# Performance work log

Hardware: AMD Instinct MI355X
Metric: run time of the kernel (lower is better)

## Reference

```python
import jax, jax.numpy as jnp
import numpy as np
from jax import lax

B, C, OUT, K, H, W = 8, 64, 32, 3, 64, 64


def _conv2d(x, w, b, stride=1, pad=0, groups=1):
    o = lax.conv_general_dilated(x, w, (stride, stride), [(pad, pad), (pad, pad)],
                                 dimension_numbers=('NCHW', 'OIHW', 'NCHW'),
                                 feature_group_count=groups)
    return o + b[None, :, None, None]


def _bn(x, g, b, m, v, eps=1e-5):
    # eval-mode BatchNorm2d with running stats
    s = g / jnp.sqrt(v + eps)
    return x * s[None, :, None, None] + (b - m * s)[None, :, None, None]


def _eca(x, w):
    # global avg pool -> 1D conv over channel axis -> sigmoid gate [b,c,1,1]
    y = x.mean((-2, -1))[:, None, :]  # [b,1,c]
    y = lax.conv_general_dilated(y, w, (1,), [(1, 1)],
                                 dimension_numbers=('NCW', 'OIW', 'NCW'))
    return jax.nn.sigmoid(y[:, 0, :])[:, :, None, None]


def _avgpool3(x):
    # AvgPool2d(k=3, stride=1, pad=1), count_include_pad=True (torch default)
    s = lax.reduce_window(x, 0.0, lax.add, (1, 1, 3, 3), (1, 1, 1, 1),
                          [(0, 0), (0, 0), (1, 1), (1, 1)])
    return s / 9.0


def _forward(x, sc_w, sc_b, ac_w, ac_b, oc_w, oc_b, oc_bn_g, oc_bn_b, oc_bn_m, oc_bn_v,
             ex_w, ey_w, ez_w, ff_w, ff_b, g1_w, g1_b, g2_w, g2_b,
             fu_w, fu_b, fu_bn_g, fu_bn_b, fu_bn_m, fu_bn_v):
    b, c, h, w = x.shape
    k = K
    # --- ReceptiveFieldAttentionConv ---
    frf = jax.nn.silu(_conv2d(x, sc_w, sc_b, pad=k // 2, groups=c))
    frf = frf.reshape(b, c, k * k, h, w)
    arf = _conv2d(_avgpool3(x), ac_w, ac_b, groups=c).reshape(b, c, k * k, h, w)
    arf = jax.nn.softmax(arf, axis=2)  # softmax over k*k RF positions
    wt = (frf * arf).reshape(b, c, k, k, h, w)
    wt = wt.transpose(0, 1, 4, 2, 5, 3).reshape(b, c, h * k, w * k)  # pixel-shuffle-like
    x_rfa = jax.nn.silu(_bn(_conv2d(wt, oc_w, oc_b, stride=k, groups=4),
                            oc_bn_g, oc_bn_b, oc_bn_m, oc_bn_v))
    # --- FrequencyGroupedChannelAttention ---
    energy = jnp.abs(jnp.fft.fft2(x)).mean((-2, -1))  # [b,c]
    ranks = jnp.argsort(jnp.argsort(-energy, axis=1), axis=1)
    mask = (ranks < c // 2).astype(x.dtype)[:, :, None, None]  # top-half-energy channels
    a_x = _eca(x, ex_w)
    a_y = _eca(x * mask, ey_w)
    a_z = _eca(x * (1.0 - mask), ez_w)
    a_f = _conv2d(jnp.concatenate([a_y, a_z], 1), ff_w, ff_b, groups=4)
    g_in = jnp.concatenate([a_f, a_x], 1)
    g = jax.nn.sigmoid(_conv2d(jax.nn.silu(_conv2d(g_in, g1_w, g1_b)), g2_w, g2_b))
    x_fgca = x * (g * a_f + (1.0 - g) * a_x)
    # --- fuse ---
    fused = jnp.concatenate([x_rfa, x_fgca], 1)
    return jax.nn.silu(_bn(_conv2d(fused, fu_w, fu_b),
                           fu_bn_g, fu_bn_b, fu_bn_m, fu_bn_v))


def setup_inputs() -> dict:
    key = jax.random.key(0)
    ks = jax.random.split(key, 32)
    rn = lambda k, shp, s=0.1: jax.random.normal(k, shp, jnp.float32) * s
    gh = max(8, C // 4)  # gate hidden = 16
    return {
        'x': jax.random.normal(ks[0], (B, C, H, W), jnp.float32),
        'sc_w': rn(ks[1], (C * K * K, 1, K, K)), 'sc_b': rn(ks[2], (C * K * K,)),
        'ac_w': rn(ks[3], (C * K * K, 1, 1, 1)), 'ac_b': rn(ks[4], (C * K * K,)),
        'oc_w': rn(ks[5], (C, C // 4, K, K)), 'oc_b': rn(ks[6], (C,)),
        'oc_bn_g': 1.0 + rn(ks[7], (C,)), 'oc_bn_b': rn(ks[8], (C,)),
        'oc_bn_m': rn(ks[9], (C,)), 'oc_bn_v': 0.9 + 0.2 * jax.random.uniform(ks[10], (C,), jnp.float32),
        'ex_w': rn(ks[11], (1, 1, 3), 0.3), 'ey_w': rn(ks[12], (1, 1, 3), 0.3),
        'ez_w': rn(ks[13], (1, 1, 3), 0.3),
        'ff_w': rn(ks[14], (C, 2 * C // 4, 1, 1)), 'ff_b': rn(ks[15], (C,)),
        'g1_w': rn(ks[16], (gh, 2 * C, 1, 1)), 'g1_b': rn(ks[17], (gh,)),
        'g2_w': rn(ks[18], (C, gh, 1, 1)), 'g2_b': rn(ks[19], (C,)),
        'fu_w': rn(ks[20], (OUT, 2 * C, 1, 1)), 'fu_b': rn(ks[21], (OUT,)),
        'fu_bn_g': 1.0 + rn(ks[22], (OUT,)), 'fu_bn_b': rn(ks[23], (OUT,)),
        'fu_bn_m': rn(ks[24], (OUT,)), 'fu_bn_v': 0.9 + 0.2 * jax.random.uniform(ks[25], (OUT,), jnp.float32),
    }


def reference(x, sc_w, sc_b, ac_w, ac_b, oc_w, oc_b, oc_bn_g, oc_bn_b, oc_bn_m, oc_bn_v,
              ex_w, ey_w, ez_w, ff_w, ff_b, g1_w, g1_b, g2_w, g2_b,
              fu_w, fu_b, fu_bn_g, fu_bn_b, fu_bn_m, fu_bn_v):
    return _forward(x, sc_w, sc_b, ac_w, ac_b, oc_w, oc_b, oc_bn_g, oc_bn_b, oc_bn_m, oc_bn_v,
                    ex_w, ey_w, ez_w, ff_w, ff_b, g1_w, g1_b, g2_w, g2_b,
                    fu_w, fu_b, fu_bn_g, fu_bn_b, fu_bn_m, fu_bn_v)
```

## Files before the change

kernel.cpp:

```cpp
#include <hip/hip_runtime.h>
#include <math.h>

#define EPS 1e-5f

__device__ __forceinline__ float wave_sum(float v) {
  v += __shfl_down(v, 32);
  v += __shfl_down(v, 16);
  v += __shfl_down(v, 8);
  v += __shfl_down(v, 4);
  v += __shfl_down(v, 2);
  v += __shfl_down(v, 1);
  return v;
}

__device__ __forceinline__ float silu_f(float v) { return v / (1.f + __expf(-v)); }
__device__ __forceinline__ float sigm_f(float v) { return 1.f / (1.f + __expf(-v)); }

__device__ __forceinline__ int bitrev6(int v) {
  return ((v & 1) << 5) | ((v & 2) << 3) | ((v & 4) << 1) |
         ((v & 8) >> 1) | ((v & 16) >> 3) | ((v & 32) >> 5);
}

#define FFT6(zr, zi)                                           \
  do {                                                         \
    _Pragma("unroll") for (int s = 0; s < 6; ++s) {            \
      const int half = 32 >> s;                                \
      const bool up = (lane & half) != 0;                      \
      float pr = __shfl_xor(zr, half);                         \
      float pi = __shfl_xor(zi, half);                         \
      float tr = up ? pr - zr : zr + pr;                       \
      float ti = up ? pi - zi : zi + pi;                       \
      const float c = twc[s], sn = tws[s];                     \
      zr = tr * c - ti * sn;                                   \
      zi = tr * sn + ti * c;                                   \
    }                                                          \
  } while (0)

__global__ __launch_bounds__(256) void k_dft(const float* __restrict__ x,
                                             float* __restrict__ energy,
                                             float* __restrict__ meanx) {
  __shared__ float re1[33 * 65];
  __shared__ float im1[33 * 65];
  __shared__ float redA[4], redB[4];
  const int bc = blockIdx.x;
  const int tid = threadIdx.x;
  const int lane = tid & 63;
  const int wv = tid >> 6;
  const float* xp = x + (size_t)bc * 4096;

  float twc[6], tws[6];
#pragma unroll
  for (int s = 0; s < 6; ++s) {
    int half = 32 >> s;
    if (lane & half) {
      float ang = -6.283185307179586f * (float)((lane & (half - 1)) << s) / 64.f;
      float sv, cv;
      __sincosf(ang, &sv, &cv);
      twc[s] = cv;
      tws[s] = sv;
    } else {
      twc[s] = 1.f;
      tws[s] = 0.f;
    }
  }

  const int f = bitrev6(lane);
  const int fm = (64 - f) & 63;
  const int plane = bitrev6(fm);

  float lsum = 0.f;
#pragma unroll 1
  for (int rp = 0; rp < 4; ++rp) {
    const int h0 = wv * 16 + rp * 4;
    float x0 = xp[h0 * 64 + lane];
    float x1 = xp[(h0 + 1) * 64 + lane];
    float x2 = xp[(h0 + 2) * 64 + lane];
    float x3 = xp[(h0 + 3) * 64 + lane];
    lsum += x0 + x1 + x2 + x3;
    float zr = x0, zi = x1, yr = x2, yi = x3;
#pragma unroll
    for (int s = 0; s < 6; ++s) {
      const int half = 32 >> s;
      const bool up = (lane & half) != 0;
      float pzr = __shfl_xor(zr, half);
      float pzi = __shfl_xor(zi, half);
      float pyr = __shfl_xor(yr, half);
      float pyi = __shfl_xor(yi, half);
      float tzr = up ? pzr - zr : zr + pzr;
      float tzi = up ? pzi - zi : zi + pzi;
      float tyr = up ? pyr - yr : yr + pyr;
      float tyi = up ? pyi - yi : yi + pyi;
      const float c = twc[s], sn = tws[s];
      zr = tzr * c - tzi * sn;
      zi = tzr * sn + tzi * c;
      yr = tyr * c - tyi * sn;
      yi = tyr * sn + tyi * c;
    }
    float mzr = __shfl(zr, plane), mzi = __shfl(zi, plane);
    float myr = __shfl(yr, plane), myi = __shfl(yi, plane);
    if (f <= 32) {
      float ar = 0.5f * (zr + mzr), ai = 0.5f * (zi - mzi);
      float br = 0.5f * (zi + mzi), bi = 0.5f * (mzr - zr);
      float cr = 0.5f * (yr + myr), ci = 0.5f * (yi - myi);
      float dr = 0.5f * (yi + myi), di = 0.5f * (myr - yr);
      re1[f * 65 + h0] = ar;     im1[f * 65 + h0] = ai;
      re1[f * 65 + h0 + 1] = br; im1[f * 65 + h0 + 1] = bi;
      re1[f * 65 + h0 + 2] = cr; im1[f * 65 + h0 + 2] = ci;
      re1[f * 65 + h0 + 3] = dr; im1[f * 65 + h0 + 3] = di;
    }
  }
  __syncthreads();

  float msum = 0.f;
#pragma unroll 1
  for (int i = 0; i < 4; ++i) {
    const int kv1 = wv + 8 * i;
    const int kv2 = kv1 + 4;
    const float w1 = (kv1 == 0) ? 1.f : 2.f;
    float ar = re1[kv1 * 65 + lane];
    float ai = im1[kv1 * 65 + lane];
    float br = re1[kv2 * 65 + lane];
    float bi = im1[kv2 * 65 + lane];
#pragma unroll
    for (int s = 0; s < 6; ++s) {
      const int half = 32 >> s;
      const bool up = (lane & half) != 0;
      float par = __shfl_xor(ar, half);
      float pai = __shfl_xor(ai, half);
      float pbr = __shfl_xor(br, half);
      float pbi = __shfl_xor(bi, half);
      float tar = up ? par - ar : ar + par;
      float tai = up ? pai - ai : ai + pai;
      float tbr = up ? pbr - br : br + pbr;
      float tbi = up ? pbi - bi : bi + pbi;
      const float c = twc[s], sn = tws[s];
      ar = tar * c - tai * sn;
      ai = tar * sn + tai * c;
      br = tbr * c - tbi * sn;
      bi = tbr * sn + tbi * c;
    }
    msum += w1 * sqrtf(ar * ar + ai * ai) + 2.f * sqrtf(br * br + bi * bi);
  }
  if (wv == 0) {
    float ar = re1[32 * 65 + lane];
    float ai = im1[32 * 65 + lane];
    FFT6(ar, ai);
    msum += sqrtf(ar * ar + ai * ai);
  }

  msum = wave_sum(msum);
  lsum = wave_sum(lsum);
  if (lane == 0) { redA[wv] = msum; redB[wv] = lsum; }
  __syncthreads();
  if (tid == 0) {
    float e = redA[0] + redA[1] + redA[2] + redA[3];
    float m = redB[0] + redB[1] + redB[2] + redB[3];
    energy[bc] = e * (1.f / 4096.f);
    meanx[bc] = m * (1.f / 4096.f);
  }
}

__global__ __launch_bounds__(64) void k_attn(
    const float* __restrict__ energy, const float* __restrict__ meanx,
    const float* __restrict__ ex_w, const float* __restrict__ ey_w,
    const float* __restrict__ ez_w, const float* __restrict__ ff_w,
    const float* __restrict__ ff_b, const float* __restrict__ g1_w,
    const float* __restrict__ g1_b, const float* __restrict__ g2_w,
    const float* __restrict__ g2_b, float* __restrict__ s2) {
  __shared__ float e[64], mx[64], my[64], mz[64];
  __shared__ float ax[64], ay[64], az[64], af[64], h1[16];
  const int b = blockIdx.x;
  const int c = threadIdx.x;
  e[c] = energy[b * 64 + c];
  mx[c] = meanx[b * 64 + c];
  __syncthreads();
  int rank = 0;
  float ec = e[c];
  for (int i = 0; i < 64; ++i) {
    float ei = e[i];
    rank += (ei > ec) || (ei == ec && i < c);
  }
  float mask = (rank < 32) ? 1.f : 0.f;
  my[c] = mx[c] * mask;
  mz[c] = mx[c] * (1.f - mask);
  __syncthreads();
  {
    float l, r, m;
    l = (c > 0) ? mx[c - 1] : 0.f; m = mx[c]; r = (c < 63) ? mx[c + 1] : 0.f;
    ax[c] = sigm_f(ex_w[0] * l + ex_w[1] * m + ex_w[2] * r);
    l = (c > 0) ? my[c - 1] : 0.f; m = my[c]; r = (c < 63) ? my[c + 1] : 0.f;
    ay[c] = sigm_f(ey_w[0] * l + ey_w[1] * m + ey_w[2] * r);
    l = (c > 0) ? mz[c - 1] : 0.f; m = mz[c]; r = (c < 63) ? mz[c + 1] : 0.f;
    az[c] = sigm_f(ez_w[0] * l + ez_w[1] * m + ez_w[2] * r);
  }
  __syncthreads();
  {
    int g = c >> 4;
    float acc = ff_b[c];
#pragma unroll
    for (int i = 0; i < 32; ++i) {
      int ch = g * 32 + i;
      float v = (ch < 64) ? ay[ch] : az[ch - 64];
      acc = fmaf(v, ff_w[c * 32 + i], acc);
    }
    af[c] = acc;
  }
  __syncthreads();
  if (c < 16) {
    float a = g1_b[c];
#pragma unroll
    for (int i = 0; i < 64; ++i) a = fmaf(af[i], g1_w[c * 128 + i], a);
#pragma unroll
    for (int i = 0; i < 64; ++i) a = fmaf(ax[i], g1_w[c * 128 + 64 + i], a);
    h1[c] = silu_f(a);
  }
  __syncthreads();
  float gv = g2_b[c];
#pragma unroll
  for (int o = 0; o < 16; ++o) gv = fmaf(h1[o], g2_w[c * 16 + o], gv);
  gv = sigm_f(gv);
  s2[b * 64 + c] = gv * af[c] + (1.f - gv) * ax[c];
}

__global__ __launch_bounds__(256) void k_rfa(
    const float* __restrict__ x,
    const float* __restrict__ sc_w, const float* __restrict__ sc_b,
    const float* __restrict__ ac_w, const float* __restrict__ ac_b,
    const float* __restrict__ oc_w, const float* __restrict__ oc_b,
    const float* __restrict__ bn_g, const float* __restrict__ bn_b,
    const float* __restrict__ bn_m, const float* __restrict__ bn_v,
    float* __restrict__ xrfa) {
  __shared__ __align__(16) float scwp[16 * 9 * 12];
  __shared__ __align__(16) float mp[16 * 24];
  __shared__ __align__(16) float ocwp[16 * 16 * 12];
  __shared__ float red[128 * 33];
  const int blk = blockIdx.x;
  const int band = blk & 15;
  const int g = (blk >> 4) & 3;
  const int b = blk >> 6;
  const int tid = threadIdx.x;
  const int lane = tid & 63;
  const int wv = tid >> 6;
  const int wp = wv & 1;
  const int half = wv >> 1;

  for (int i = tid; i < 1296; i += 256) {
    int icg = i / 81, rem = i - icg * 81;
    int j = rem / 9, t = rem - j * 9;
    scwp[icg * 108 + j * 12 + t] = sc_w[(g * 144 + icg * 9 + j) * 9 + t];
  }
  if (tid < 144) {
    int icg = tid / 9, j = tid - icg * 9;
    scwp[icg * 108 + j * 12 + 9] = sc_b[g * 144 + tid];
    mp[icg * 24 + j] = ac_w[g * 144 + tid];
    mp[icg * 24 + 12 + j] = ac_b[g * 144 + tid];
  }
  for (int i = tid; i < 2304; i += 256) {
    int oco = i / 144, rem = i - oco * 144;
    int icg = rem / 9, j = rem - icg * 9;
    ocwp[icg * 192 + oco * 12 + j] = oc_w[((g * 16 + oco) * 16 + icg) * 9 + j];
  }
  __syncthreads();

  const int r0 = band * 4 + wp * 2;
  const int w = lane;
  const bool vW = w > 0, vE = w < 63;
  float acc0[16], acc1[16];
#pragma unroll
  for (int i = 0; i < 16; ++i) { acc0[i] = 0.f; acc1[i] = 0.f; }

  const float* xg = x + ((size_t)(b * 64 + g * 16)) * 4096 + w;
  const int icg0 = half * 8;

#pragma unroll 1
  for (int ii = 0; ii < 8; ++ii) {
    const int icg = icg0 + ii;
    const float* xc = xg + icg * 4096;
    float n[12];
#pragma unroll
    for (int t = 0; t < 4; ++t) {
      int h = r0 - 1 + t;
      bool vh = (h >= 0) && (h < 64);
      const float* row = xc + h * 64;
      n[t * 3 + 0] = (vh && vW) ? row[-1] : 0.f;
      n[t * 3 + 1] = vh ? row[0] : 0.f;
      n[t * 3 + 2] = (vh && vE) ? row[1] : 0.f;
    }
    float rs0 = n[0] + n[1] + n[2];
    float rs1 = n[3] + n[4] + n[5];
    float rs2 = n[6] + n[7] + n[8];
    float rs3 = n[9] + n[10] + n[11];
    float ap0 = (rs0 + rs1 + rs2) * (1.f / 9.f);
    float ap1 = (rs1 + rs2 + rs3) * (1.f / 9.f);

    float aw[12], ab[12];
    *(float4*)&aw[0] = *(const float4*)&mp[icg * 24];
    *(float4*)&aw[4] = *(const float4*)&mp[icg * 24 + 4];
    *(float4*)&aw[8] = *(const float4*)&mp[icg * 24 + 8];
    *(float4*)&ab[0] = *(const float4*)&mp[icg * 24 + 12];
    *(float4*)&ab[4] = *(const float4*)&mp[icg * 24 + 16];
    *(float4*)&ab[8] = *(const float4*)&mp[icg * 24 + 20];

    float f0[9], f1[9], a0[9], a1[9];
    float amax0 = -1e30f, amax1 = -1e30f;
#pragma unroll
    for (int j = 0; j < 9; ++j) {
      float wt[12];
      *(float4*)&wt[0] = *(const float4*)&scwp[icg * 108 + j * 12];
      *(float4*)&wt[4] = *(const float4*)&scwp[icg * 108 + j * 12 + 4];
      *(float4*)&wt[8] = *(const float4*)&scwp[icg * 108 + j * 12 + 8];
      float p0 = wt[9], p1 = wt[9];
#pragma unroll
      for (int t = 0; t < 9; ++t) {
        p0 = fmaf(n[t], wt[t], p0);
        p1 = fmaf(n[t + 3], wt[t], p1);
      }
      f0[j] = silu_f(p0);
      f1[j] = silu_f(p1);
      float v0 = fmaf(ap0, aw[j], ab[j]);
      float v1 = fmaf(ap1, aw[j], ab[j]);
      a0[j] = v0; a1[j] = v1;
      amax0 = fmaxf(amax0, v0);
      amax1 = fmaxf(amax1, v1);
    }
    float es0 = 0.f, es1 = 0.f;
    float p0[9], p1[9];
#pragma unroll
    for (int j = 0; j < 9; ++j) {
      float e0 = __expf(a0[j] - amax0);
      float e1 = __expf(a1[j] - amax1);
      es0 += e0; es1 += e1;
      p0[j] = f0[j] * e0;
      p1[j] = f1[j] * e1;
    }
    float i0 = __fdividef(1.f, es0);
    float i1 = __fdividef(1.f, es1);
#pragma unroll
    for (int j = 0; j < 9; ++j) { p0[j] *= i0; p1[j] *= i1; }

#pragma unroll
    for (int oco = 0; oco < 16; ++oco) {
      float ov[12];
      *(float4*)&ov[0] = *(const float4*)&ocwp[icg * 192 + oco * 12];
      *(float4*)&ov[4] = *(const float4*)&ocwp[icg * 192 + oco * 12 + 4];
      *(float4*)&ov[8] = *(const float4*)&ocwp[icg * 192 + oco * 12 + 8];
      float s0 = 0.f, s1 = 0.f;
#pragma unroll
      for (int j = 0; j < 9; ++j) {
        s0 = fmaf(p0[j], ov[j], s0);
        s1 = fmaf(p1[j], ov[j], s1);
      }
      acc0[oco] += s0;
      acc1[oco] += s1;
    }
  }

  const int rid = wp * 64 + lane;
  if (half == 1) {
#pragma unroll
    for (int k = 0; k < 16; ++k) {
      red[rid * 33 + k] = acc0[k];
      red[rid * 33 + 16 + k] = acc1[k];
    }
  }
  __syncthreads();
  if (half == 0) {
#pragma unroll
    for (int k = 0; k < 16; ++k) {
      acc0[k] += red[rid * 33 + k];
      acc1[k] += red[rid * 33 + 16 + k];
    }
    float* op = xrfa + ((size_t)(b * 64 + g * 16)) * 4096 + r0 * 64 + w;
#pragma unroll
    for (int oco = 0; oco < 16; ++oco) {
      int oc = g * 16 + oco;
      float s = bn_g[oc] * rsqrtf(bn_v[oc] + EPS);
      float bb = bn_b[oc] - bn_m[oc] * s;
      float ob = oc_b[oc];
      float v0 = fmaf(acc0[oco] + ob, s, bb);
      float v1 = fmaf(acc1[oco] + ob, s, bb);
      op[oco * 4096] = silu_f(v0);
      op[oco * 4096 + 64] = silu_f(v1);
    }
  }
}

__global__ __launch_bounds__(256) void k_fuse(
    const float* __restrict__ x, const float* __restrict__ xrfa,
    const float* __restrict__ s2, const float* __restrict__ fu_w,
    const float* __restrict__ fu_b, const float* __restrict__ bn_g,
    const float* __restrict__ bn_b, const float* __restrict__ bn_m,
    const float* __restrict__ bn_v, float* __restrict__ out) {
  __shared__ __align__(16) float fw[4096];
  __shared__ float s2l[64];
  const int blk = blockIdx.x;
  const int tid = threadIdx.x;
  const int sloc = tid & 63;
  const int ocq = tid >> 6;
  const int b = blk >> 6;
  const int sp = (blk & 63) * 64 + sloc;

  for (int i = tid; i < 1024; i += 256)
    ((float4*)fw)[i] = ((const float4*)fu_w)[i];
  if (tid < 64) s2l[tid] = s2[b * 64 + tid];

  const float* xr = xrfa + (size_t)b * 64 * 4096 + sp;
  const float* xp = x + (size_t)b * 64 * 4096 + sp;
  float va[64], vb[64];
#pragma unroll
  for (int i = 0; i < 64; ++i) va[i] = xr[i * 4096];
#pragma unroll
  for (int i = 0; i < 64; ++i) vb[i] = xp[i * 4096];
  __syncthreads();
#pragma unroll
  for (int i = 0; i < 64; ++i) vb[i] *= s2l[i];

  float* op = out + (size_t)b * 32 * 4096 + sp;
#pragma unroll 1
  for (int o = 0; o < 8; ++o) {
    const int oc = ocq * 8 + o;
    const float* wr = &fw[oc * 128];
    float a = 0.f;
#pragma unroll
    for (int q = 0; q < 16; ++q) {
      float4 w4 = *(const float4*)&wr[q * 4];
      a = fmaf(va[q * 4 + 0], w4.x, a);
      a = fmaf(va[q * 4 + 1], w4.y, a);
      a = fmaf(va[q * 4 + 2], w4.z, a);
      a = fmaf(va[q * 4 + 3], w4.w, a);
    }
#pragma unroll
    for (int q = 0; q < 16; ++q) {
      float4 w4 = *(const float4*)&wr[64 + q * 4];
      a = fmaf(vb[q * 4 + 0], w4.x, a);
      a = fmaf(vb[q * 4 + 1], w4.y, a);
      a = fmaf(vb[q * 4 + 2], w4.z, a);
      a = fmaf(vb[q * 4 + 3], w4.w, a);
    }
    float s = bn_g[oc] * rsqrtf(bn_v[oc] + EPS);
    float v = a + fu_b[oc];
    v = fmaf(v, s, bn_b[oc] - bn_m[oc] * s);
    op[oc * 4096] = silu_f(v);
  }
}

extern "C" void kernel_launch(void* const* d_in, const int* in_sizes, int n_in,
                              void* d_out, int out_size, void* d_ws, size_t ws_size,
                              hipStream_t stream) {
  const float* x       = (const float*)d_in[0];
  const float* sc_w    = (const float*)d_in[1];
  const float* sc_b    = (const float*)d_in[2];
  const float* ac_w    = (const float*)d_in[3];
  const float* ac_b    = (const float*)d_in[4];
  const float* oc_w    = (const float*)d_in[5];
  const float* oc_b    = (const float*)d_in[6];
  const float* oc_bn_g = (const float*)d_in[7];
  const float* oc_bn_b = (const float*)d_in[8];
  const float* oc_bn_m = (const float*)d_in[9];
  const float* oc_bn_v = (const float*)d_in[10];
  const float* ex_w    = (const float*)d_in[11];
  const float* ey_w    = (const float*)d_in[12];
  const float* ez_w    = (const float*)d_in[13];
  const float* ff_w    = (const float*)d_in[14];
  const float* ff_b    = (const float*)d_in[15];
  const float* g1_w    = (const float*)d_in[16];
  const float* g1_b    = (const float*)d_in[17];
  const float* g2_w    = (const float*)d_in[18];
  const float* g2_b    = (const float*)d_in[19];
  const float* fu_w    = (const float*)d_in[20];
  const float* fu_b    = (const float*)d_in[21];
  const float* fu_bn_g = (const float*)d_in[22];
  const float* fu_bn_b = (const float*)d_in[23];
  const float* fu_bn_m = (const float*)d_in[24];
  const float* fu_bn_v = (const float*)d_in[25];

  float* ws     = (float*)d_ws;
  float* energy = ws;
  float* meanx  = ws + 512;
  float* s2     = ws + 1024;
  float* xrfa   = ws + 2048;

  k_dft<<<512, 256, 0, stream>>>(x, energy, meanx);
  k_attn<<<8, 64, 0, stream>>>(energy, meanx, ex_w, ey_w, ez_w,
                               ff_w, ff_b, g1_w, g1_b, g2_w, g2_b, s2);
  k_rfa<<<512, 256, 0, stream>>>(x, sc_w, sc_b, ac_w, ac_b, oc_w, oc_b,
                                 oc_bn_g, oc_bn_b, oc_bn_m, oc_bn_v, xrfa);
  k_fuse<<<512, 256, 0, stream>>>(x, xrfa, s2, fu_w, fu_b,
                                  fu_bn_g, fu_bn_b, fu_bn_m, fu_bn_v,
                                  (float*)d_out);
}
```

Baseline: 174.1 us.

## Split RFA kernel work across four waves per channel group with LDS atomic reduction

The RFA kernel now uses 1024 blocks, each covering two output rows instead of four. All four waves handle both rows, and each wave takes a quarter of the 16 input channels instead of half. Partial sums are combined with shared-memory atomics into a zeroed buffer, then two waves finish the rows. This is meant to raise parallelism and occupancy. The cost is that weight staging into LDS runs twice as often, and the atomic reduction and buffer clear add overhead.

```diff
diff --git a/kernel.cpp b/kernel.cpp
--- a/kernel.cpp
+++ b/kernel.cpp
@@ -233,16 +233,14 @@
   __shared__ __align__(16) float scwp[16 * 9 * 12];
   __shared__ __align__(16) float mp[16 * 24];
   __shared__ __align__(16) float ocwp[16 * 16 * 12];
-  __shared__ float red[128 * 33];
+  __shared__ float mbuf[128 * 33];
   const int blk = blockIdx.x;
-  const int band = blk & 15;
-  const int g = (blk >> 4) & 3;
-  const int b = blk >> 6;
+  const int band = blk & 31;
+  const int g = (blk >> 5) & 3;
+  const int b = blk >> 7;
   const int tid = threadIdx.x;
   const int lane = tid & 63;
   const int wv = tid >> 6;
-  const int wp = wv & 1;
-  const int half = wv >> 1;
 
   for (int i = tid; i < 1296; i += 256) {
     int icg = i / 81, rem = i - icg * 81;
@@ -260,9 +258,10 @@
     int icg = rem / 9, j = rem - icg * 9;
     ocwp[icg * 192 + oco * 12 + j] = oc_w[((g * 16 + oco) * 16 + icg) * 9 + j];
   }
-  __syncthreads();
-
-  const int r0 = band * 4 + wp * 2;
+  for (int i = tid; i < 128 * 33; i += 256) mbuf[i] = 0.f;
+  __syncthreads();
+
+  const int r0 = band * 2;
   const int w = lane;
   const bool vW = w > 0, vE = w < 63;
   float acc0[16], acc1[16];
@@ -270,10 +269,10 @@
   for (int i = 0; i < 16; ++i) { acc0[i] = 0.f; acc1[i] = 0.f; }
 
   const float* xg = x + ((size_t)(b * 64 + g * 16)) * 4096 + w;
-  const int icg0 = half * 8;
+  const int icg0 = wv * 4;
 
 #pragma unroll 1
-  for (int ii = 0; ii < 8; ++ii) {
+  for (int ii = 0; ii < 4; ++ii) {
     const int icg = icg0 + ii;
     const float* xc = xg + icg * 4096;
     float n[12];
@@ -355,32 +354,37 @@
     }
   }
 
-  const int rid = wp * 64 + lane;
-  if (half == 1) {
-#pragma unroll
-    for (int k = 0; k < 16; ++k) {
-      red[rid * 33 + k] = acc0[k];
-      red[rid * 33 + 16 + k] = acc1[k];
-    }
-  }
-  __syncthreads();
-  if (half == 0) {
-#pragma unroll
-    for (int k = 0; k < 16; ++k) {
-      acc0[k] += red[rid * 33 + k];
-      acc1[k] += red[rid * 33 + 16 + k];
-    }
-    float* op = xrfa + ((size_t)(b * 64 + g * 16)) * 4096 + r0 * 64 + w;
+  if (wv != 0) {
+    float* rp = &mbuf[lane * 33];
+#pragma unroll
+    for (int k = 0; k < 16; ++k) atomicAdd(&rp[k], acc0[k]);
+  }
+  if (wv != 1) {
+    float* rp = &mbuf[(64 + lane) * 33];
+#pragma unroll
+    for (int k = 0; k < 16; ++k) atomicAdd(&rp[k], acc1[k]);
+  }
+  __syncthreads();
+
+  if (wv < 2) {
+    float av[16];
+    if (wv == 0) {
+      const float* rp = &mbuf[lane * 33];
+#pragma unroll
+      for (int k = 0; k < 16; ++k) av[k] = acc0[k] + rp[k];
+    } else {
+      const float* rp = &mbuf[(64 + lane) * 33];
+#pragma unroll
+      for (int k = 0; k < 16; ++k) av[k] = acc1[k] + rp[k];
+    }
+    float* op = xrfa + ((size_t)(b * 64 + g * 16)) * 4096 + (r0 + wv) * 64 + w;
 #pragma unroll
     for (int oco = 0; oco < 16; ++oco) {
       int oc = g * 16 + oco;
       float s = bn_g[oc] * rsqrtf(bn_v[oc] + EPS);
       float bb = bn_b[oc] - bn_m[oc] * s;
-      float ob = oc_b[oc];
-      float v0 = fmaf(acc0[oco] + ob, s, bb);
-      float v1 = fmaf(acc1[oco] + ob, s, bb);
-      op[oco * 4096] = silu_f(v0);
-      op[oco * 4096 + 64] = silu_f(v1);
+      float v = fmaf(av[oco] + oc_b[oc], s, bb);
+      op[oco * 4096] = silu_f(v);
     }
   }
 }
@@ -483,8 +487,8 @@
   k_dft<<<512, 256, 0, stream>>>(x, energy, meanx);
   k_attn<<<8, 64, 0, stream>>>(energy, meanx, ex_w, ey_w, ez_w,
                                ff_w, ff_b, g1_w, g1_b, g2_w, g2_b, s2);
-  k_rfa<<<512, 256, 0, stream>>>(x, sc_w, sc_b, ac_w, ac_b, oc_w, oc_b,
-                                 oc_bn_g, oc_bn_b, oc_bn_m, oc_bn_v, xrfa);
+  k_rfa<<<1024, 256, 0, stream>>>(x, sc_w, sc_b, ac_w, ac_b, oc_w, oc_b,
+                                  oc_bn_g, oc_bn_b, oc_bn_m, oc_bn_v, xrfa);
   k_fuse<<<512, 256, 0, stream>>>(x, xrfa, s2, fu_w, fu_b,
                                   fu_bn_g, fu_bn_b, fu_bn_m, fu_bn_v,
                                   (float*)d_out);
```

Result: slower. 200.7 us (+15.3%).
